# Kernel optimization log

Measured on AMD Instinct MI355X. Metric: run time of the kernel, lower is better.

The kernel has to match this reference:

```python
import jax, jax.numpy as jnp
import numpy as np
from jax import lax

B, N, CIN, COUT, NPOINT, K = 8, 4096, 64, 128, 1024, 24
EPS = 1e-5


def setup_inputs() -> dict:
    key = jax.random.key(0)
    ks = jax.random.split(key, 16)
    def conv_w(k, o, i):
        return jax.random.normal(k, (o, i), jnp.float32) * (1.0 / np.sqrt(i))
    inp = {
        "xyz": jax.random.normal(ks[0], (B, N, 3), jnp.float32),
        "x": jax.random.normal(ks[1], (B, CIN, N), jnp.float32),
        "farthest0": jax.random.randint(ks[2], (B,), 0, N),
        # Local.proj: Conv1DBR (CIN -> COUT, k=1, no bias)
        "W_proj": conv_w(ks[3], COUT, CIN), "g_proj": jnp.ones(COUT), "b_proj": jnp.zeros(COUT),
        # Local.channel: one Conv1DBRRes (COUT -> COUT -> COUT)
        "W_la1": conv_w(ks[4], COUT, COUT), "g_la1": jnp.ones(COUT), "b_la1": jnp.zeros(COUT),
        "W_la2": conv_w(ks[5], COUT, COUT), "g_la2": jnp.ones(COUT), "b_la2": jnp.zeros(COUT),
        # ca: one Conv1DBRRes (COUT -> COUT -> COUT)
        "W_ca1": conv_w(ks[6], COUT, COUT), "g_ca1": jnp.ones(COUT), "b_ca1": jnp.zeros(COUT),
        "W_ca2": conv_w(ks[7], COUT, COUT), "g_ca2": jnp.ones(COUT), "b_ca2": jnp.zeros(COUT),
    }
    return inp


def _bn(z, g, b):
    # BatchNorm1d in training mode: biased batch stats over (batch, length)
    mu = z.mean((0, 2), keepdims=True)
    var = z.var((0, 2), keepdims=True)
    return g[None, :, None] * (z - mu) * lax.rsqrt(var + EPS) + b[None, :, None]


def _conv(z, W):  # kernel_size=1 Conv1d == channel matmul
    return jnp.einsum('oc,mcl->mol', W, z)


def _resblock(z, W1, g1, b1, W2, g2, b2):
    y = jax.nn.relu(_bn(_conv(z, W1), g1, b1))
    y = _bn(_conv(y, W2), g2, b2)
    return jax.nn.relu(y + z)


def _forward(xyz, x, farthest0,
             W_proj, g_proj, b_proj,
             W_la1, g_la1, b_la1, W_la2, g_la2, b_la2,
             W_ca1, g_ca1, b_ca1, W_ca2, g_ca2, b_ca2):
    Bv, Nv, _ = xyz.shape
    xt = jnp.transpose(x, (0, 2, 1))  # [B, N, C]

    # --- farthest point sampling (sequential, vectorized over batch) ---
    def step(carry, _):
        dist, far = carry
        c = jnp.take_along_axis(xyz, far[:, None, None], axis=1)  # [B,1,3]
        d = jnp.sum((xyz - c) ** 2, -1)                           # [B,N]
        dist = jnp.minimum(dist, d)
        return (dist, jnp.argmax(dist, -1)), far

    init = (jnp.full((Bv, Nv), 1e10, xyz.dtype), farthest0)
    _, cent = lax.scan(step, init, None, length=NPOINT)
    fps_idx = cent.T  # [B, NPOINT]

    new_xyz = jnp.take_along_axis(xyz, fps_idx[:, :, None], axis=1)  # [B,NP,3]
    new_pts = jnp.take_along_axis(xt, fps_idx[:, :, None], axis=1)   # [B,NP,C]

    # --- kNN grouping: squared distances [B, NP, N], smallest-K indices ---
    d2 = (jnp.sum(new_xyz ** 2, -1)[:, :, None]
          + jnp.sum(xyz ** 2, -1)[:, None, :]
          - 2.0 * jnp.einsum('bpc,bnc->bpn', new_xyz, xyz))
    _, knn = lax.top_k(-d2, K)  # [B, NP, K]
    grouped = jax.vmap(lambda p, i: p[i])(xt, knn)  # [B, NP, K, C]
    edge = grouped - new_pts[:, :, None, :]         # [B, NP, K, C]

    # --- Local: per-group conv-BN-ReLU + residual block + max over K ---
    M = Bv * NPOINT
    h = jnp.transpose(edge, (0, 1, 3, 2)).reshape(M, edge.shape[-1], K)  # [M, CIN, K]
    h = jax.nn.relu(_bn(_conv(h, W_proj), g_proj, b_proj))
    h = _resblock(h, W_la1, g_la1, b_la1, W_la2, g_la2, b_la2)
    h = h.max(-1)  # adaptive_max_pool1d(.,1) -> [M, COUT]
    h = h.reshape(Bv, NPOINT, -1).transpose(0, 2, 1)  # [B, COUT, NP]

    # --- Channel (ca) ---
    h = _resblock(h, W_ca1, g_ca1, b_ca1, W_ca2, g_ca2, b_ca2)
    return new_xyz, h


def reference(xyz, x, farthest0,
              W_proj, g_proj, b_proj,
              W_la1, g_la1, b_la1, W_la2, g_la2, b_la2,
              W_ca1, g_ca1, b_ca1, W_ca2, g_ca2, b_ca2):
    return _forward(xyz, x, farthest0,
                    W_proj, g_proj, b_proj,
                    W_la1, g_la1, b_la1, W_la2, g_la2, b_la2,
                    W_ca1, g_ca1, b_ca1, W_ca2, g_ca2, b_ca2)
```

## Files before the change

kernel.cpp:

```cpp
#include <hip/hip_runtime.h>

#define BB 8
#define NN 4096
#define CIN 64
#define COUTC 128
#define NPT 1024
#define KNN 24

typedef unsigned short u16;
typedef unsigned int u32;
typedef unsigned long long u64;

using short8v = __attribute__((ext_vector_type(8))) short;
using f32x4  = __attribute__((ext_vector_type(4))) float;
using f32x2  = __attribute__((ext_vector_type(2))) float;

__device__ __forceinline__ u16 f2bf(float f){ u32 u=__float_as_uint(f); u += 0x7FFFu + ((u>>16)&1u); return (u16)(u>>16); }
__device__ __forceinline__ float bf2f(u16 h){ return __uint_as_float(((u32)h)<<16); }

template<int C> __device__ __forceinline__ float dppmax_f32(float x){
  int y=__builtin_amdgcn_update_dpp(__float_as_int(x),__float_as_int(x),C,0xF,0xF,false);
  return fmaxf(x,__int_as_float(y));
}
template<int C> __device__ __forceinline__ u32 dppmin_u32(u32 x){
  u32 y=(u32)__builtin_amdgcn_update_dpp((int)x,(int)x,C,0xF,0xF,false);
  return y<x?y:x;
}
__device__ __forceinline__ f32x2 vmin2(f32x2 a, f32x2 b){
#if __has_builtin(__builtin_elementwise_min)
  return __builtin_elementwise_min(a,b);
#else
  f32x2 r; r.x=fminf(a.x,b.x); r.y=fminf(a.y,b.y); return r;
#endif
}
__device__ __forceinline__ f32x2 vmax2(f32x2 a, f32x2 b){
#if __has_builtin(__builtin_elementwise_max)
  return __builtin_elementwise_max(a,b);
#else
  f32x2 r; r.x=fmaxf(a.x,b.x); r.y=fmaxf(a.y,b.y); return r;
#endif
}

__global__ __launch_bounds__(256) void xt_kern(const float* __restrict__ x, float* __restrict__ xt,
                                               const float* __restrict__ xyz, float* __restrict__ sn){
  __shared__ float tile[64][68];
  int blk=blockIdx.x; int b=blk>>6; int n0=(blk&63)<<6;
  int t=threadIdx.x;
  {
    int c=t>>2, nj=(t&3)*16;
    const float4* gp=reinterpret_cast<const float4*>(x + ((size_t)(b*64+c))*NN + n0+nj);
    #pragma unroll
    for(int j=0;j<4;j++){
      float4 v=gp[j];
      *reinterpret_cast<float4*>(&tile[c][nj+4*j])=v;
    }
  }
  if(t<64){
    int n=n0+t;
    const float* p=xyz+((size_t)b*NN+n)*3;
    float xx=p[0], yy=p[1], zz=p[2];
    sn[b*NN+n]=__fadd_rn(__fadd_rn(__fmul_rn(xx,xx),__fmul_rn(yy,yy)),__fmul_rn(zz,zz));
  }
  __syncthreads();
  {
    int n=t>>2, c16=(t&3)*16;
    size_t base=((size_t)(b*NN+n0+n))*64 + c16;
    #pragma unroll
    for(int j=0;j<4;j++){
      *reinterpret_cast<float4*>(xt+base+4*j)=
        make_float4(tile[c16+4*j][n],tile[c16+4*j+1][n],tile[c16+4*j+2][n],tile[c16+4*j+3][n]);
    }
  }
}

__global__ __launch_bounds__(256) void fps_kern(const float* __restrict__ xyz,
    const int* __restrict__ far0, int* __restrict__ fps_idx)
{
  __shared__ float4 lp[NN];
  __shared__ u64 mkey[2][4];
  const int b=blockIdx.x, t=threadIdx.x, w=t>>6, l=t&63;
  f32x2 px2[8],py2[8],pz2[8],d2v[8];
  {
    float4 q[12];
    const float4* gp=reinterpret_cast<const float4*>(xyz+(size_t)b*NN*3)+(size_t)t*12;
    #pragma unroll
    for(int i=0;i<12;i++) q[i]=gp[i];
    const float* v=reinterpret_cast<const float*>(q);
    #pragma unroll
    for(int j=0;j<8;j++){
      px2[j]=(f32x2){v[6*j+0],v[6*j+3]};
      py2[j]=(f32x2){v[6*j+1],v[6*j+4]};
      pz2[j]=(f32x2){v[6*j+2],v[6*j+5]};
      lp[t*16+2*j  ]=make_float4(v[6*j+0],v[6*j+1],v[6*j+2],0.f);
      lp[t*16+2*j+1]=make_float4(v[6*j+3],v[6*j+4],v[6*j+5],0.f);
      d2v[j]=(f32x2){1e10f,1e10f};
    }
  }
  __syncthreads();
  int far=far0[b];
  float4 c=lp[far];
  int par=0;
  for(int it=0;it<NPT;++it){
    if(t==0) fps_idx[b*NPT+it]=far;
    f32x2 cx2=(f32x2){c.x,c.x}, cy2=(f32x2){c.y,c.y}, cz2=(f32x2){c.z,c.z};
    f32x2 m2=(f32x2){-1.f,-1.f};
    #pragma unroll
    for(int j=0;j<8;j++){
      f32x2 dx=px2[j]-cx2, dy=py2[j]-cy2, dz=pz2[j]-cz2;
      f32x2 d=(dx*dx+dy*dy)+dz*dz;
      f32x2 nd=vmin2(d2v[j],d); d2v[j]=nd;
      m2=vmax2(m2,nd);
    }
    float m0=fmaxf(m2.x,m2.y);
    if(it==NPT-1) break;
    float r=m0;
    r=dppmax_f32<0x111>(r); r=dppmax_f32<0x112>(r); r=dppmax_f32<0x114>(r);
    r=dppmax_f32<0x118>(r); r=dppmax_f32<0x142>(r); r=dppmax_f32<0x143>(r);
    float wmax=__int_as_float(__builtin_amdgcn_readlane(__float_as_int(r),63));
    u64 bal=__ballot(m0==wmax);
    int winlane=__ffsll((unsigned long long)bal)-1;
    int myj=15;
    #pragma unroll
    for(int j=7;j>=0;--j){
      if(d2v[j].y==m0) myj=2*j+1;
      if(d2v[j].x==m0) myj=2*j;
    }
    int widx_w=__builtin_amdgcn_readlane(t*16+myj,winlane);
    if(l==0) mkey[par][w]=(((u64)__float_as_uint(wmax))<<32)|(u32)(~(u32)widx_w);
    asm volatile("s_waitcnt lgkmcnt(0)\n\ts_barrier" ::: "memory");
    u64 k4=mkey[par][l&3];
    u32 klo=(u32)k4, khi=(u32)(k4>>32);
    {
      u32 nlo=(u32)__builtin_amdgcn_update_dpp((int)klo,(int)klo,0xB1,0xF,0xF,false);
      u32 nhi=(u32)__builtin_amdgcn_update_dpp((int)khi,(int)khi,0xB1,0xF,0xF,false);
      bool g=(nhi>khi)||((nhi==khi)&&(nlo>klo));
      klo=g?nlo:klo; khi=g?nhi:khi;
    }
    {
      u32 nlo=(u32)__builtin_amdgcn_update_dpp((int)klo,(int)klo,0x4E,0xF,0xF,false);
      u32 nhi=(u32)__builtin_amdgcn_update_dpp((int)khi,(int)khi,0x4E,0xF,0xF,false);
      bool g=(nhi>khi)||((nhi==khi)&&(nlo>klo));
      klo=g?nlo:klo; khi=g?nhi:khi;
    }
    int widx=(int)(~klo);
    far=widx;
    c=lp[widx];
    par^=1;
  }
}

__global__ __launch_bounds__(256) void knn_kern(const float* __restrict__ xyz,
  const float* __restrict__ sn, const int* __restrict__ fps,
  const float* __restrict__ xt, u16* __restrict__ edge, float* __restrict__ outxyz)
{
  __shared__ u64 mkey[2][4];
  __shared__ int sel[KNN];
  const int m=blockIdx.x, b=m>>10;
  const int t=threadIdx.x, w=t>>6, l=t&63;
  const int ctr=fps[m];
  const float sp=sn[b*NN+ctr];
  float cx,cy,cz;
  { const float* cp=xyz+((size_t)b*NN+ctr)*3; cx=cp[0]; cy=cp[1]; cz=cp[2]; }
  u32 key[16];
  {
    float4 q[12];
    const float4* gp=reinterpret_cast<const float4*>(xyz+((size_t)b*NN)*3+(size_t)t*48);
    #pragma unroll
    for(int i=0;i<12;i++) q[i]=gp[i];
    const float* v=reinterpret_cast<const float*>(q);
    float snl[16];
    const float4* sp4=reinterpret_cast<const float4*>(sn+b*NN+t*16);
    #pragma unroll
    for(int i=0;i<4;i++){ float4 s4=sp4[i]; snl[4*i]=s4.x; snl[4*i+1]=s4.y; snl[4*i+2]=s4.z; snl[4*i+3]=s4.w; }
    #pragma unroll
    for(int j=0;j<16;j++){
      float nx=v[3*j], ny=v[3*j+1], nz=v[3*j+2];
      float dot=__fadd_rn(__fadd_rn(__fmul_rn(cx,nx),__fmul_rn(cy,ny)),__fmul_rn(cz,nz));
      float d2=__fsub_rn(__fadd_rn(sp,snl[j]),__fmul_rn(2.f,dot));
      u32 bbv=__float_as_uint(d2);
      key[j]=(bbv&0x80000000u)?~bbv:(bbv|0x80000000u);
    }
  }
  u32 loc=0xFFFFFFFFu; int myj=0;
  #pragma unroll
  for(int j=15;j>=0;--j){ if(key[j]<=loc){ loc=key[j]; myj=j; } }
  int par=0;
  for(int rd=0;rd<KNN;rd++){
    u32 r=loc;
    r=dppmin_u32<0x111>(r); r=dppmin_u32<0x112>(r); r=dppmin_u32<0x114>(r);
    r=dppmin_u32<0x118>(r); r=dppmin_u32<0x142>(r); r=dppmin_u32<0x143>(r);
    u32 wmin=(u32)__builtin_amdgcn_readlane((int)r,63);
    u64 bal=__ballot(loc==wmin);
    int winlane=__ffsll((unsigned long long)bal)-1;
    int widx_w=__builtin_amdgcn_readlane(t*16+myj,winlane);
    if(l==0) mkey[par][w]=(((u64)wmin)<<32)|(u32)widx_w;
    asm volatile("s_waitcnt lgkmcnt(0)\n\ts_barrier" ::: "memory");
    u64 b0=mkey[par][0],b1=mkey[par][1],b2=mkey[par][2],b3=mkey[par][3];
    u64 bb0=b0<b1?b0:b1, bb1=b2<b3?b2:b3, best=bb0<bb1?bb0:bb1;
    int widx=(int)(u32)(best&0xFFFFFFFFull);
    if(t==(widx>>4)){
      key[widx&15]=0xFFFFFFFFu;
      loc=0xFFFFFFFFu; myj=0;
      #pragma unroll
      for(int j=15;j>=0;--j){ if(key[j]<=loc){ loc=key[j]; myj=j; } }
    }
    if(t==0) sel[rd]=widx;
    par^=1;
  }
  if(t<3) outxyz[(size_t)m*3+t]=xyz[((size_t)b*NN+ctr)*3+t];
  __syncthreads();
  {
    int r=t>>3, c0=(t&7)*8;
    if(r<KNN){
      int nb=sel[r];
      const float* np_=xt+((size_t)b*NN+nb)*64+c0;
      const float* cp_=xt+((size_t)b*NN+ctr)*64+c0;
      float4 n0=*reinterpret_cast<const float4*>(np_);
      float4 n1=*reinterpret_cast<const float4*>(np_+4);
      float4 c0v=*reinterpret_cast<const float4*>(cp_);
      float4 c1v=*reinterpret_cast<const float4*>(cp_+4);
      u32 ov[4];
      ov[0]=(u32)f2bf(__fsub_rn(n0.x,c0v.x))|((u32)f2bf(__fsub_rn(n0.y,c0v.y))<<16);
      ov[1]=(u32)f2bf(__fsub_rn(n0.z,c0v.z))|((u32)f2bf(__fsub_rn(n0.w,c0v.w))<<16);
      ov[2]=(u32)f2bf(__fsub_rn(n1.x,c1v.x))|((u32)f2bf(__fsub_rn(n1.y,c1v.y))<<16);
      ov[3]=(u32)f2bf(__fsub_rn(n1.z,c1v.z))|((u32)f2bf(__fsub_rn(n1.w,c1v.w))<<16);
      *reinterpret_cast<uint4*>(edge+((size_t)m*KNN+r)*64+c0)=make_uint4(ov[0],ov[1],ov[2],ov[3]);
    }
  }
}

template<int KD, bool XF>
__global__ __launch_bounds__(256) void gemm_bn(
    const u16* __restrict__ A, const float* __restrict__ W,
    const float* __restrict__ af, const float* __restrict__ cf,
    u16* __restrict__ Z, float* __restrict__ pSum, float* __restrict__ pSq,
    int nblk4)
{
  extern __shared__ char smem[];
  u16* lA=(u16*)smem;
  u16* lW=lA+128*KD;
  const int t=threadIdx.x, blk=blockIdx.x;
  constexpr int TPR=KD/8;
  constexpr int RPP=256/TPR;
  constexpr int NPASS=128/RPP;
  const int rl=t/TPR, c0=(t%TPR)*8;
  float ax[8], cxx[8];
  if constexpr (XF){
    #pragma unroll
    for(int j=0;j<8;j++){ ax[j]=af[c0+j]; cxx[j]=cf[c0+j]; }
  }
  #pragma unroll
  for(int p=0;p<NPASS;p++){
    int row=p*RPP+rl;
    uint4 v=*reinterpret_cast<const uint4*>(A+((size_t)blk*128+row)*KD+c0);
    if constexpr (XF){
      u32 in[4]={v.x,v.y,v.z,v.w}; u32 out[4];
      #pragma unroll
      for(int q2=0;q2<4;q2++){
        float f0=__uint_as_float((in[q2]&0xFFFFu)<<16);
        float f1=__uint_as_float(in[q2]&0xFFFF0000u);
        f0=fmaxf(fmaf(ax[2*q2],f0,cxx[2*q2]),0.f);
        f1=fmaxf(fmaf(ax[2*q2+1],f1,cxx[2*q2+1]),0.f);
        out[q2]=(u32)f2bf(f0)|((u32)f2bf(f1)<<16);
      }
      v.x=out[0]; v.y=out[1]; v.z=out[2]; v.w=out[3];
    }
    int byte=row*(KD*2)+c0*2; byte^=(row&7)<<4;
    *reinterpret_cast<uint4*>((char*)lA+byte)=v;
    const float* wp_=W+(size_t)row*KD+c0;
    float4 w0=*reinterpret_cast<const float4*>(wp_);
    float4 w1=*reinterpret_cast<const float4*>(wp_+4);
    uint4 wv;
    wv.x=(u32)f2bf(w0.x)|((u32)f2bf(w0.y)<<16);
    wv.y=(u32)f2bf(w0.z)|((u32)f2bf(w0.w)<<16);
    wv.z=(u32)f2bf(w1.x)|((u32)f2bf(w1.y)<<16);
    wv.w=(u32)f2bf(w1.z)|((u32)f2bf(w1.w)<<16);
    int wbyte=row*(KD*2)+c0*2; wbyte^=(row&7)<<4;
    *reinterpret_cast<uint4*>((char*)lW+wbyte)=wv;
  }
  __syncthreads();
  const int l=t&63, w2=t>>6;
  const int l15=l&15, qq=l>>4;
  f32x4 acc[2][8];
  #pragma unroll
  for(int r=0;r<2;r++)
    #pragma unroll
    for(int f=0;f<8;f++) acc[r][f]=(f32x4){0.f,0.f,0.f,0.f};
  #pragma unroll
  for(int s=0;s<KD/32;s++){
    short8v a[2];
    #pragma unroll
    for(int r=0;r<2;r++){
      int row=w2*32+r*16+l15;
      int byte=row*(KD*2)+s*64+qq*16; byte^=(row&7)<<4;
      a[r]=*reinterpret_cast<const short8v*>((char*)lA+byte);
    }
    #pragma unroll
    for(int f=0;f<8;f++){
      int row=f*16+l15;
      int byte=row*(KD*2)+s*64+qq*16; byte^=(row&7)<<4;
      short8v bb=*reinterpret_cast<const short8v*>((char*)lW+byte);
      acc[0][f]=__builtin_amdgcn_mfma_f32_16x16x32_bf16(a[0],bb,acc[0][f],0,0,0);
      acc[1][f]=__builtin_amdgcn_mfma_f32_16x16x32_bf16(a[1],bb,acc[1][f],0,0,0);
    }
  }
  #pragma unroll
  for(int f=0;f<8;f++){
    float sv=0.f,qv=0.f;
    #pragma unroll
    for(int r=0;r<2;r++){
      int grow=blk*128+w2*32+r*16+qq*4;
      #pragma unroll
      for(int j=0;j<4;j++){
        float v=acc[r][f][j];
        Z[((size_t)(grow+j))*128+f*16+l15]=f2bf(v);
        sv+=v; qv+=v*v;
      }
    }
    sv+=__shfl_xor(sv,16); sv+=__shfl_xor(sv,32);
    qv+=__shfl_xor(qv,16); qv+=__shfl_xor(qv,32);
    if(l<16){
      int col=f*16+l15;
      pSum[(size_t)col*nblk4+blk*4+w2]=sv;
      pSq [(size_t)col*nblk4+blk*4+w2]=qv;
    }
  }
}

__global__ __launch_bounds__(256) void stats_kern(
  const float* __restrict__ pSum, const float* __restrict__ pSq,
  const float* __restrict__ g, const float* __restrict__ bb,
  float* __restrict__ af, float* __restrict__ cf, int nparts, float inv_cnt)
{
  int ch=blockIdx.x, t=threadIdx.x;
  float s=0.f,q=0.f;
  for(int i=t;i<nparts;i+=256){ s+=pSum[(size_t)ch*nparts+i]; q+=pSq[(size_t)ch*nparts+i]; }
  #pragma unroll
  for(int o=1;o<64;o<<=1){ s+=__shfl_xor(s,o); q+=__shfl_xor(q,o); }
  __shared__ float ls[4], lq[4];
  int w=t>>6, l=t&63;
  if(l==0){ ls[w]=s; lq[w]=q; }
  __syncthreads();
  if(t==0){
    float S=ls[0]+ls[1]+ls[2]+ls[3], Q=lq[0]+lq[1]+lq[2]+lq[3];
    float mu=S*inv_cnt, var=Q*inv_cnt-mu*mu;
    float a=g[ch]/sqrtf(var+1e-5f);
    af[ch]=a; cf[ch]=bb[ch]-mu*a;
  }
}

__global__ __launch_bounds__(256) void pool_kern(const u16* __restrict__ z3, const u16* __restrict__ z1,
  const float* __restrict__ af1, const float* __restrict__ cf1,
  const float* __restrict__ af3, const float* __restrict__ cf3, u16* __restrict__ pooled)
{
  int t=threadIdx.x;
  int g=blockIdx.x*2+(t>>7);
  int c=t&127;
  float a1=af1[c],c1=cf1[c],a3=af3[c],c3=cf3[c];
  float mmax=0.f;
  size_t base=(size_t)g*KNN*128+c;
  #pragma unroll 4
  for(int k=0;k<KNN;k++){
    float v3=bf2f(z3[base+(size_t)k*128]);
    float v1=bf2f(z1[base+(size_t)k*128]);
    float z1p=fmaxf(fmaf(a1,v1,c1),0.f);
    float v=fmaf(a3,v3,c3)+z1p;
    mmax=fmaxf(mmax,fmaxf(v,0.f));
  }
  pooled[(size_t)g*128+c]=f2bf(mmax);
}

__global__ __launch_bounds__(256) void final_kern(const u16* __restrict__ z5,
  const u16* __restrict__ pooled, const float* __restrict__ af, const float* __restrict__ cf,
  float* __restrict__ outh)
{
  __shared__ float tile[64][68];
  int blk=blockIdx.x; int b=blk>>5; int tl=blk&31; int p0=(tl&15)<<6; int o0=(tl>>4)<<6;
  int t=threadIdx.x;
  {
    int pl=t>>2, o1=(t&3)*16;
    size_t base=((size_t)(b*1024+p0+pl))*128 + o0+o1;
    #pragma unroll
    for(int h2=0;h2<2;h2++){
      uint4 v5=*reinterpret_cast<const uint4*>(z5+base+h2*8);
      uint4 vp=*reinterpret_cast<const uint4*>(pooled+base+h2*8);
      u32 a5[4]={v5.x,v5.y,v5.z,v5.w}; u32 pp[4]={vp.x,vp.y,vp.z,vp.w};
      #pragma unroll
      for(int q2=0;q2<4;q2++){
        int oj=o1+h2*8+q2*2;
        float g0=af[o0+oj],h0=cf[o0+oj],g1=af[o0+oj+1],h1=cf[o0+oj+1];
        float f0=__uint_as_float((a5[q2]&0xFFFFu)<<16);
        float f1=__uint_as_float(a5[q2]&0xFFFF0000u);
        float q0=__uint_as_float((pp[q2]&0xFFFFu)<<16);
        float q1=__uint_as_float(pp[q2]&0xFFFF0000u);
        tile[oj][pl]  =fmaxf(fmaf(g0,f0,h0)+q0,0.f);
        tile[oj+1][pl]=fmaxf(fmaf(g1,f1,h1)+q1,0.f);
      }
    }
  }
  __syncthreads();
  {
    int ol=t>>2, pj=(t&3)*16;
    size_t obase=((size_t)(b*128+o0+ol))*1024 + p0+pj;
    #pragma unroll
    for(int j=0;j<4;j++){
      *reinterpret_cast<float4*>(outh+obase+4*j)=
        make_float4(tile[ol][pj+4*j],tile[ol][pj+4*j+1],tile[ol][pj+4*j+2],tile[ol][pj+4*j+3]);
    }
  }
}

extern "C" void kernel_launch(void* const* d_in, const int* in_sizes, int n_in,
                              void* d_out, int out_size, void* d_ws, size_t ws_size,
                              hipStream_t stream)
{
  (void)in_sizes; (void)n_in; (void)out_size; (void)ws_size;
  const float* xyz   =(const float*)d_in[0];
  const float* x     =(const float*)d_in[1];
  const int*   far0  =(const int*)d_in[2];
  const float* W_proj=(const float*)d_in[3];
  const float* g_proj=(const float*)d_in[4];
  const float* b_proj=(const float*)d_in[5];
  const float* W_la1 =(const float*)d_in[6];
  const float* g_la1 =(const float*)d_in[7];
  const float* b_la1 =(const float*)d_in[8];
  const float* W_la2 =(const float*)d_in[9];
  const float* g_la2 =(const float*)d_in[10];
  const float* b_la2 =(const float*)d_in[11];
  const float* W_ca1 =(const float*)d_in[12];
  const float* g_ca1 =(const float*)d_in[13];
  const float* b_ca1 =(const float*)d_in[14];
  const float* W_ca2 =(const float*)d_in[15];
  const float* g_ca2 =(const float*)d_in[16];
  const float* b_ca2 =(const float*)d_in[17];

  char* ws=(char*)d_ws;
  const size_t OFF_XT =0;
  const size_t OFF_SN =8388608;
  const size_t OFF_FPS=8519680;
  const size_t OFF_AF =8552448;
  const size_t OFF_CF =8555008;
  const size_t OFF_PS =8557568;
  const size_t OFF_PQ =11703296;
  const size_t OFF_PL =14849024;
  const size_t OFF_Z4 =16946176;
  const size_t OFF_Z5 =19043328;
  const size_t OFF_Z1 =21140480;
  const size_t OFF_B2 =71472128;

  float* xt  =(float*)(ws+OFF_XT);
  float* sn  =(float*)(ws+OFF_SN);
  int* fps   =(int*)(ws+OFF_FPS);
  float* af  =(float*)(ws+OFF_AF);
  float* cf  =(float*)(ws+OFF_CF);
  float* pS  =(float*)(ws+OFF_PS);
  float* pQ  =(float*)(ws+OFF_PQ);
  u16* pooled=(u16*)(ws+OFF_PL);
  u16* z4    =(u16*)(ws+OFF_Z4);
  u16* z5    =(u16*)(ws+OFF_Z5);
  u16* z1    =(u16*)(ws+OFF_Z1);
  u16* edge  =(u16*)(ws+OFF_B2);
  u16* z2    =(u16*)(ws+OFF_B2);
  u16* z3    =(u16*)(ws+OFF_B2);
  float* outxyz=(float*)d_out;
  float* outh  =(float*)d_out+24576;

  const float invL=1.f/196608.f, invC=1.f/8192.f;

  xt_kern<<<512,256,0,stream>>>(x,xt,xyz,sn);
  fps_kern<<<8,256,0,stream>>>(xyz,far0,fps);
  knn_kern<<<8192,256,0,stream>>>(xyz,sn,fps,xt,edge,outxyz);

  gemm_bn<64,false><<<1536,256,32768,stream>>>(edge,W_proj,nullptr,nullptr,z1,pS,pQ,6144);
  stats_kern<<<128,256,0,stream>>>(pS,pQ,g_proj,b_proj,af+0,cf+0,6144,invL);

  gemm_bn<128,true><<<1536,256,65536,stream>>>(z1,W_la1,af+0,cf+0,z2,pS,pQ,6144);
  stats_kern<<<128,256,0,stream>>>(pS,pQ,g_la1,b_la1,af+128,cf+128,6144,invL);

  gemm_bn<128,true><<<1536,256,65536,stream>>>(z2,W_la2,af+128,cf+128,z3,pS,pQ,6144);
  stats_kern<<<128,256,0,stream>>>(pS,pQ,g_la2,b_la2,af+256,cf+256,6144,invL);

  pool_kern<<<4096,256,0,stream>>>(z3,z1,af+0,cf+0,af+256,cf+256,pooled);

  gemm_bn<128,false><<<64,256,65536,stream>>>(pooled,W_ca1,nullptr,nullptr,z4,pS,pQ,256);
  stats_kern<<<128,256,0,stream>>>(pS,pQ,g_ca1,b_ca1,af+384,cf+384,256,invC);

  gemm_bn<128,true><<<64,256,65536,stream>>>(z4,W_ca2,af+384,cf+384,z5,pS,pQ,256);
  stats_kern<<<128,256,0,stream>>>(pS,pQ,g_ca2,b_ca2,af+512,cf+512,256,invC);

  final_kern<<<256,256,0,stream>>>(z5,pooled,af+512,cf+512,outh);
}
```

Measured before the change: 835.3 us.

## Merge transpose into FPS launch and make kNN selection barrier-free per wave

The transpose/norm kernel and the FPS kernel are merged into one launch. FPS runs in blocks 0-7 and the transpose tiles in the remaining blocks, reusing FPS's shared array as the tile. In kNN, each wave independently extracts its own top-24 candidates without a block barrier per round. A final merge step then ranks the 4x24 candidates by binary search to pick the global top-24. This removes 24 block-wide barriers per kNN block and one kernel launch, at the cost of each wave doing 24 rounds regardless and an extra merge phase.

```diff
diff --git a/kernel.cpp b/kernel.cpp
--- a/kernel.cpp
+++ b/kernel.cpp
@@ -41,44 +41,44 @@
 #endif
 }
 
-__global__ __launch_bounds__(256) void xt_kern(const float* __restrict__ x, float* __restrict__ xt,
-                                               const float* __restrict__ xyz, float* __restrict__ sn){
-  __shared__ float tile[64][68];
-  int blk=blockIdx.x; int b=blk>>6; int n0=(blk&63)<<6;
-  int t=threadIdx.x;
-  {
-    int c=t>>2, nj=(t&3)*16;
-    const float4* gp=reinterpret_cast<const float4*>(x + ((size_t)(b*64+c))*NN + n0+nj);
-    #pragma unroll
-    for(int j=0;j<4;j++){
-      float4 v=gp[j];
-      *reinterpret_cast<float4*>(&tile[c][nj+4*j])=v;
-    }
-  }
-  if(t<64){
-    int n=n0+t;
-    const float* p=xyz+((size_t)b*NN+n)*3;
-    float xx=p[0], yy=p[1], zz=p[2];
-    sn[b*NN+n]=__fadd_rn(__fadd_rn(__fmul_rn(xx,xx),__fmul_rn(yy,yy)),__fmul_rn(zz,zz));
-  }
-  __syncthreads();
-  {
-    int n=t>>2, c16=(t&3)*16;
-    size_t base=((size_t)(b*NN+n0+n))*64 + c16;
-    #pragma unroll
-    for(int j=0;j<4;j++){
-      *reinterpret_cast<float4*>(xt+base+4*j)=
-        make_float4(tile[c16+4*j][n],tile[c16+4*j+1][n],tile[c16+4*j+2][n],tile[c16+4*j+3][n]);
-    }
-  }
-}
-
-__global__ __launch_bounds__(256) void fps_kern(const float* __restrict__ xyz,
+__global__ __launch_bounds__(256) void pre_kern(const float* __restrict__ x, float* __restrict__ xt,
+    const float* __restrict__ xyz, float* __restrict__ sn,
     const int* __restrict__ far0, int* __restrict__ fps_idx)
 {
   __shared__ float4 lp[NN];
   __shared__ u64 mkey[2][4];
-  const int b=blockIdx.x, t=threadIdx.x, w=t>>6, l=t&63;
+  const int t=threadIdx.x;
+  if(blockIdx.x>=8){
+    float (*tile)[68]=reinterpret_cast<float(*)[68]>(lp);
+    int blk=blockIdx.x-8; int b=blk>>6; int n0=(blk&63)<<6;
+    {
+      int c=t>>2, nj=(t&3)*16;
+      const float4* gp=reinterpret_cast<const float4*>(x + ((size_t)(b*64+c))*NN + n0+nj);
+      #pragma unroll
+      for(int j=0;j<4;j++){
+        float4 v=gp[j];
+        *reinterpret_cast<float4*>(&tile[c][nj+4*j])=v;
+      }
+    }
+    if(t<64){
+      int n=n0+t;
+      const float* p=xyz+((size_t)b*NN+n)*3;
+      float xx=p[0], yy=p[1], zz=p[2];
+      sn[b*NN+n]=__fadd_rn(__fadd_rn(__fmul_rn(xx,xx),__fmul_rn(yy,yy)),__fmul_rn(zz,zz));
+    }
+    __syncthreads();
+    {
+      int n=t>>2, c16=(t&3)*16;
+      size_t base=((size_t)(b*NN+n0+n))*64 + c16;
+      #pragma unroll
+      for(int j=0;j<4;j++){
+        *reinterpret_cast<float4*>(xt+base+4*j)=
+          make_float4(tile[c16+4*j][n],tile[c16+4*j+1][n],tile[c16+4*j+2][n],tile[c16+4*j+3][n]);
+      }
+    }
+    return;
+  }
+  const int b=blockIdx.x, w=t>>6, l=t&63;
   f32x2 px2[8],py2[8],pz2[8],d2v[8];
   {
     float4 q[12];
@@ -153,7 +153,8 @@
   const float* __restrict__ sn, const int* __restrict__ fps,
   const float* __restrict__ xt, u16* __restrict__ edge, float* __restrict__ outxyz)
 {
-  __shared__ u64 mkey[2][4];
+  __shared__ u32 ckey[4][KNN];
+  __shared__ int cidx[4][KNN];
   __shared__ int sel[KNN];
   const int m=blockIdx.x, b=m>>10;
   const int t=threadIdx.x, w=t>>6, l=t&63;
@@ -184,7 +185,6 @@
   u32 loc=0xFFFFFFFFu; int myj=0;
   #pragma unroll
   for(int j=15;j>=0;--j){ if(key[j]<=loc){ loc=key[j]; myj=j; } }
-  int par=0;
   for(int rd=0;rd<KNN;rd++){
     u32 r=loc;
     r=dppmin_u32<0x111>(r); r=dppmin_u32<0x112>(r); r=dppmin_u32<0x114>(r);
@@ -193,19 +193,31 @@
     u64 bal=__ballot(loc==wmin);
     int winlane=__ffsll((unsigned long long)bal)-1;
     int widx_w=__builtin_amdgcn_readlane(t*16+myj,winlane);
-    if(l==0) mkey[par][w]=(((u64)wmin)<<32)|(u32)widx_w;
-    asm volatile("s_waitcnt lgkmcnt(0)\n\ts_barrier" ::: "memory");
-    u64 b0=mkey[par][0],b1=mkey[par][1],b2=mkey[par][2],b3=mkey[par][3];
-    u64 bb0=b0<b1?b0:b1, bb1=b2<b3?b2:b3, best=bb0<bb1?bb0:bb1;
-    int widx=(int)(u32)(best&0xFFFFFFFFull);
-    if(t==(widx>>4)){
-      key[widx&15]=0xFFFFFFFFu;
+    if(l==winlane){
+      key[myj]=0xFFFFFFFFu;
       loc=0xFFFFFFFFu; myj=0;
       #pragma unroll
       for(int j=15;j>=0;--j){ if(key[j]<=loc){ loc=key[j]; myj=j; } }
     }
-    if(t==0) sel[rd]=widx;
-    par^=1;
+    if(l==0){ ckey[w][rd]=wmin; cidx[w][rd]=widx_w; }
+  }
+  __syncthreads();
+  if(t<96){
+    int wl=t/24, i=t-wl*24;
+    u32 k=ckey[wl][i]; int idx=cidx[wl][i];
+    int rank=i;
+    #pragma unroll
+    for(int ww=0;ww<4;ww++){
+      if(ww==wl) continue;
+      int lo=0,hi=KNN;
+      while(lo<hi){ int mid=(lo+hi)>>1;
+        u32 k2=ckey[ww][mid]; int i2=cidx[ww][mid];
+        bool less=(k2<k)||(k2==k&&i2<idx);
+        if(less) lo=mid+1; else hi=mid;
+      }
+      rank+=lo;
+    }
+    if(rank<KNN) sel[rank]=idx;
   }
   if(t<3) outxyz[(size_t)m*3+t]=xyz[((size_t)b*NN+ctr)*3+t];
   __syncthreads();
@@ -467,8 +479,7 @@
 
   const float invL=1.f/196608.f, invC=1.f/8192.f;
 
-  xt_kern<<<512,256,0,stream>>>(x,xt,xyz,sn);
-  fps_kern<<<8,256,0,stream>>>(xyz,far0,fps);
+  pre_kern<<<520,256,0,stream>>>(x,xt,xyz,sn,far0,fps);
   knn_kern<<<8192,256,0,stream>>>(xyz,sn,fps,xt,edge,outxyz);
 
   gemm_bn<64,false><<<1536,256,32768,stream>>>(edge,W_proj,nullptr,nullptr,z1,pS,pQ,6144);
```

Result: slower. 892.6 us (+6.9%).

## Fuse transpose, FPS and kNN into one persistent kernel with flag-based overlap

Applied to the files above, without the earlier changes.

Merges the transpose/norm, farthest point sampling and kNN/edge-gather kernels into one 512-block launch. Eight blocks run FPS and publish each sampled index through an atomic store. The other 504 worker blocks first do the transpose, meet at a global atomic barrier, then spin on per-sample flags so kNN for early centroids overlaps with the sequential FPS. This hides the kNN work behind the long serial FPS chain, at the cost of spin-waiting, two extra memsets, and relying on all 512 blocks being resident at once.

```diff
diff --git a/kernel.cpp b/kernel.cpp
--- a/kernel.cpp
+++ b/kernel.cpp
@@ -6,6 +6,7 @@
 #define COUTC 128
 #define NPT 1024
 #define KNN 24
+#define NWRK 504
 
 typedef unsigned short u16;
 typedef unsigned int u32;
@@ -41,44 +42,139 @@
 #endif
 }
 
-__global__ __launch_bounds__(256) void xt_kern(const float* __restrict__ x, float* __restrict__ xt,
-                                               const float* __restrict__ xyz, float* __restrict__ sn){
-  __shared__ float tile[64][68];
-  int blk=blockIdx.x; int b=blk>>6; int n0=(blk&63)<<6;
-  int t=threadIdx.x;
-  {
-    int c=t>>2, nj=(t&3)*16;
-    const float4* gp=reinterpret_cast<const float4*>(x + ((size_t)(b*64+c))*NN + n0+nj);
-    #pragma unroll
-    for(int j=0;j<4;j++){
-      float4 v=gp[j];
-      *reinterpret_cast<float4*>(&tile[c][nj+4*j])=v;
-    }
-  }
-  if(t<64){
-    int n=n0+t;
-    const float* p=xyz+((size_t)b*NN+n)*3;
-    float xx=p[0], yy=p[1], zz=p[2];
-    sn[b*NN+n]=__fadd_rn(__fadd_rn(__fmul_rn(xx,xx),__fmul_rn(yy,yy)),__fmul_rn(zz,zz));
-  }
-  __syncthreads();
-  {
-    int n=t>>2, c16=(t&3)*16;
-    size_t base=((size_t)(b*NN+n0+n))*64 + c16;
-    #pragma unroll
-    for(int j=0;j<4;j++){
-      *reinterpret_cast<float4*>(xt+base+4*j)=
-        make_float4(tile[c16+4*j][n],tile[c16+4*j+1][n],tile[c16+4*j+2][n],tile[c16+4*j+3][n]);
-    }
-  }
-}
-
-__global__ __launch_bounds__(256) void fps_kern(const float* __restrict__ xyz,
-    const int* __restrict__ far0, int* __restrict__ fps_idx)
+__global__ __launch_bounds__(256) void pre_kern(const float* __restrict__ x, float* __restrict__ xt,
+    const float* __restrict__ xyz, float* __restrict__ sn,
+    const int* __restrict__ far0, int* fps_idx, int* sync,
+    u16* __restrict__ edge, float* __restrict__ outxyz)
 {
   __shared__ float4 lp[NN];
   __shared__ u64 mkey[2][4];
-  const int b=blockIdx.x, t=threadIdx.x, w=t>>6, l=t&63;
+  __shared__ int sel[KNN];
+  __shared__ int bcast;
+  const int t=threadIdx.x;
+  if(blockIdx.x>=8){
+    const int blk0=blockIdx.x-8;
+    float (*tile)[68]=reinterpret_cast<float(*)[68]>(lp);
+    for(int tl=blk0; tl<512; tl+=NWRK){
+      int b=tl>>6, n0=(tl&63)<<6;
+      {
+        int c=t>>2, nj=(t&3)*16;
+        const float4* gp=reinterpret_cast<const float4*>(x + ((size_t)(b*64+c))*NN + n0+nj);
+        #pragma unroll
+        for(int j=0;j<4;j++){
+          float4 v=gp[j];
+          *reinterpret_cast<float4*>(&tile[c][nj+4*j])=v;
+        }
+      }
+      if(t<64){
+        int n=n0+t;
+        const float* p=xyz+((size_t)b*NN+n)*3;
+        float xx=p[0], yy=p[1], zz=p[2];
+        sn[b*NN+n]=__fadd_rn(__fadd_rn(__fmul_rn(xx,xx),__fmul_rn(yy,yy)),__fmul_rn(zz,zz));
+      }
+      __syncthreads();
+      {
+        int n=t>>2, c16=(t&3)*16;
+        size_t base=((size_t)(b*NN+n0+n))*64 + c16;
+        #pragma unroll
+        for(int j=0;j<4;j++){
+          *reinterpret_cast<float4*>(xt+base+4*j)=
+            make_float4(tile[c16+4*j][n],tile[c16+4*j+1][n],tile[c16+4*j+2][n],tile[c16+4*j+3][n]);
+        }
+      }
+      __syncthreads();
+    }
+    if(t==0){
+      __hip_atomic_fetch_add(sync,1,__ATOMIC_RELEASE,__HIP_MEMORY_SCOPE_AGENT);
+      while(__hip_atomic_load(sync,__ATOMIC_ACQUIRE,__HIP_MEMORY_SCOPE_AGENT)<NWRK)
+        __builtin_amdgcn_s_sleep(8);
+    }
+    __syncthreads();
+    const int w=t>>6, l=t&63;
+    for(int m=blk0; m<8192; m+=NWRK){
+      if(t==0){
+        int v;
+        while((v=__hip_atomic_load(&fps_idx[m],__ATOMIC_RELAXED,__HIP_MEMORY_SCOPE_AGENT))<0)
+          __builtin_amdgcn_s_sleep(8);
+        bcast=v;
+      }
+      __syncthreads();
+      const int ctr=bcast;
+      const int b=m>>10;
+      const float sp=sn[b*NN+ctr];
+      float cx,cy,cz;
+      { const float* cp=xyz+((size_t)b*NN+ctr)*3; cx=cp[0]; cy=cp[1]; cz=cp[2]; }
+      u32 key[16];
+      {
+        float4 q[12];
+        const float4* gp=reinterpret_cast<const float4*>(xyz+((size_t)b*NN)*3+(size_t)t*48);
+        #pragma unroll
+        for(int i=0;i<12;i++) q[i]=gp[i];
+        const float* v=reinterpret_cast<const float*>(q);
+        float snl[16];
+        const float4* sp4=reinterpret_cast<const float4*>(sn+b*NN+t*16);
+        #pragma unroll
+        for(int i=0;i<4;i++){ float4 s4=sp4[i]; snl[4*i]=s4.x; snl[4*i+1]=s4.y; snl[4*i+2]=s4.z; snl[4*i+3]=s4.w; }
+        #pragma unroll
+        for(int j=0;j<16;j++){
+          float nx=v[3*j], ny=v[3*j+1], nz=v[3*j+2];
+          float dot=__fadd_rn(__fadd_rn(__fmul_rn(cx,nx),__fmul_rn(cy,ny)),__fmul_rn(cz,nz));
+          float d2=__fsub_rn(__fadd_rn(sp,snl[j]),__fmul_rn(2.f,dot));
+          u32 bbv=__float_as_uint(d2);
+          key[j]=(bbv&0x80000000u)?~bbv:(bbv|0x80000000u);
+        }
+      }
+      u32 loc=0xFFFFFFFFu; int myj=0;
+      #pragma unroll
+      for(int j=15;j>=0;--j){ if(key[j]<=loc){ loc=key[j]; myj=j; } }
+      int par=0;
+      for(int rd=0;rd<KNN;rd++){
+        u32 r=loc;
+        r=dppmin_u32<0x111>(r); r=dppmin_u32<0x112>(r); r=dppmin_u32<0x114>(r);
+        r=dppmin_u32<0x118>(r); r=dppmin_u32<0x142>(r); r=dppmin_u32<0x143>(r);
+        u32 wmin=(u32)__builtin_amdgcn_readlane((int)r,63);
+        u64 bal=__ballot(loc==wmin);
+        int winlane=__ffsll((unsigned long long)bal)-1;
+        int widx_w=__builtin_amdgcn_readlane(t*16+myj,winlane);
+        if(l==0) mkey[par][w]=(((u64)wmin)<<32)|(u32)widx_w;
+        asm volatile("s_waitcnt lgkmcnt(0)\n\ts_barrier" ::: "memory");
+        u64 b0=mkey[par][0],b1=mkey[par][1],b2=mkey[par][2],b3=mkey[par][3];
+        u64 bb0=b0<b1?b0:b1, bb1=b2<b3?b2:b3, best=bb0<bb1?bb0:bb1;
+        int widx=(int)(u32)(best&0xFFFFFFFFull);
+        if(t==(widx>>4)){
+          key[widx&15]=0xFFFFFFFFu;
+          loc=0xFFFFFFFFu; myj=0;
+          #pragma unroll
+          for(int j=15;j>=0;--j){ if(key[j]<=loc){ loc=key[j]; myj=j; } }
+        }
+        if(t==0) sel[rd]=widx;
+        par^=1;
+      }
+      if(t<3) outxyz[(size_t)m*3+t]=xyz[((size_t)b*NN+ctr)*3+t];
+      __syncthreads();
+      {
+        int r2=t>>3, c0=(t&7)*8;
+        if(r2<KNN){
+          int nb=sel[r2];
+          const float* np_=xt+((size_t)b*NN+nb)*64+c0;
+          const float* cp_=xt+((size_t)b*NN+ctr)*64+c0;
+          float4 n0=*reinterpret_cast<const float4*>(np_);
+          float4 n1=*reinterpret_cast<const float4*>(np_+4);
+          float4 c0v=*reinterpret_cast<const float4*>(cp_);
+          float4 c1v=*reinterpret_cast<const float4*>(cp_+4);
+          u32 ov[4];
+          ov[0]=(u32)f2bf(__fsub_rn(n0.x,c0v.x))|((u32)f2bf(__fsub_rn(n0.y,c0v.y))<<16);
+          ov[1]=(u32)f2bf(__fsub_rn(n0.z,c0v.z))|((u32)f2bf(__fsub_rn(n0.w,c0v.w))<<16);
+          ov[2]=(u32)f2bf(__fsub_rn(n1.x,c1v.x))|((u32)f2bf(__fsub_rn(n1.y,c1v.y))<<16);
+          ov[3]=(u32)f2bf(__fsub_rn(n1.z,c1v.z))|((u32)f2bf(__fsub_rn(n1.w,c1v.w))<<16);
+          *reinterpret_cast<uint4*>(edge+((size_t)m*KNN+r2)*64+c0)=make_uint4(ov[0],ov[1],ov[2],ov[3]);
+        }
+      }
+      __syncthreads();
+    }
+    return;
+  }
+  const int b=blockIdx.x, w=t>>6, l=t&63;
   f32x2 px2[8],py2[8],pz2[8],d2v[8];
   {
     float4 q[12];
@@ -101,7 +197,7 @@
   float4 c=lp[far];
   int par=0;
   for(int it=0;it<NPT;++it){
-    if(t==0) fps_idx[b*NPT+it]=far;
+    if(t==0) __hip_atomic_store(&fps_idx[b*NPT+it],far,__ATOMIC_RELAXED,__HIP_MEMORY_SCOPE_AGENT);
     f32x2 cx2=(f32x2){c.x,c.x}, cy2=(f32x2){c.y,c.y}, cz2=(f32x2){c.z,c.z};
     f32x2 m2=(f32x2){-1.f,-1.f};
     #pragma unroll
@@ -146,86 +242,6 @@
     far=widx;
     c=lp[widx];
     par^=1;
-  }
-}
-
-__global__ __launch_bounds__(256) void knn_kern(const float* __restrict__ xyz,
-  const float* __restrict__ sn, const int* __restrict__ fps,
-  const float* __restrict__ xt, u16* __restrict__ edge, float* __restrict__ outxyz)
-{
-  __shared__ u64 mkey[2][4];
-  __shared__ int sel[KNN];
-  const int m=blockIdx.x, b=m>>10;
-  const int t=threadIdx.x, w=t>>6, l=t&63;
-  const int ctr=fps[m];
-  const float sp=sn[b*NN+ctr];
-  float cx,cy,cz;
-  { const float* cp=xyz+((size_t)b*NN+ctr)*3; cx=cp[0]; cy=cp[1]; cz=cp[2]; }
-  u32 key[16];
-  {
-    float4 q[12];
-    const float4* gp=reinterpret_cast<const float4*>(xyz+((size_t)b*NN)*3+(size_t)t*48);
-    #pragma unroll
-    for(int i=0;i<12;i++) q[i]=gp[i];
-    const float* v=reinterpret_cast<const float*>(q);
-    float snl[16];
-    const float4* sp4=reinterpret_cast<const float4*>(sn+b*NN+t*16);
-    #pragma unroll
-    for(int i=0;i<4;i++){ float4 s4=sp4[i]; snl[4*i]=s4.x; snl[4*i+1]=s4.y; snl[4*i+2]=s4.z; snl[4*i+3]=s4.w; }
-    #pragma unroll
-    for(int j=0;j<16;j++){
-      float nx=v[3*j], ny=v[3*j+1], nz=v[3*j+2];
-      float dot=__fadd_rn(__fadd_rn(__fmul_rn(cx,nx),__fmul_rn(cy,ny)),__fmul_rn(cz,nz));
-      float d2=__fsub_rn(__fadd_rn(sp,snl[j]),__fmul_rn(2.f,dot));
-      u32 bbv=__float_as_uint(d2);
-      key[j]=(bbv&0x80000000u)?~bbv:(bbv|0x80000000u);
-    }
-  }
-  u32 loc=0xFFFFFFFFu; int myj=0;
-  #pragma unroll
-  for(int j=15;j>=0;--j){ if(key[j]<=loc){ loc=key[j]; myj=j; } }
-  int par=0;
-  for(int rd=0;rd<KNN;rd++){
-    u32 r=loc;
-    r=dppmin_u32<0x111>(r); r=dppmin_u32<0x112>(r); r=dppmin_u32<0x114>(r);
-    r=dppmin_u32<0x118>(r); r=dppmin_u32<0x142>(r); r=dppmin_u32<0x143>(r);
-    u32 wmin=(u32)__builtin_amdgcn_readlane((int)r,63);
-    u64 bal=__ballot(loc==wmin);
-    int winlane=__ffsll((unsigned long long)bal)-1;
-    int widx_w=__builtin_amdgcn_readlane(t*16+myj,winlane);
-    if(l==0) mkey[par][w]=(((u64)wmin)<<32)|(u32)widx_w;
-    asm volatile("s_waitcnt lgkmcnt(0)\n\ts_barrier" ::: "memory");
-    u64 b0=mkey[par][0],b1=mkey[par][1],b2=mkey[par][2],b3=mkey[par][3];
-    u64 bb0=b0<b1?b0:b1, bb1=b2<b3?b2:b3, best=bb0<bb1?bb0:bb1;
-    int widx=(int)(u32)(best&0xFFFFFFFFull);
-    if(t==(widx>>4)){
-      key[widx&15]=0xFFFFFFFFu;
-      loc=0xFFFFFFFFu; myj=0;
-      #pragma unroll
-      for(int j=15;j>=0;--j){ if(key[j]<=loc){ loc=key[j]; myj=j; } }
-    }
-    if(t==0) sel[rd]=widx;
-    par^=1;
-  }
-  if(t<3) outxyz[(size_t)m*3+t]=xyz[((size_t)b*NN+ctr)*3+t];
-  __syncthreads();
-  {
-    int r=t>>3, c0=(t&7)*8;
-    if(r<KNN){
-      int nb=sel[r];
-      const float* np_=xt+((size_t)b*NN+nb)*64+c0;
-      const float* cp_=xt+((size_t)b*NN+ctr)*64+c0;
-      float4 n0=*reinterpret_cast<const float4*>(np_);
-      float4 n1=*reinterpret_cast<const float4*>(np_+4);
-      float4 c0v=*reinterpret_cast<const float4*>(cp_);
-      float4 c1v=*reinterpret_cast<const float4*>(cp_+4);
-      u32 ov[4];
-      ov[0]=(u32)f2bf(__fsub_rn(n0.x,c0v.x))|((u32)f2bf(__fsub_rn(n0.y,c0v.y))<<16);
-      ov[1]=(u32)f2bf(__fsub_rn(n0.z,c0v.z))|((u32)f2bf(__fsub_rn(n0.w,c0v.w))<<16);
-      ov[2]=(u32)f2bf(__fsub_rn(n1.x,c1v.x))|((u32)f2bf(__fsub_rn(n1.y,c1v.y))<<16);
-      ov[3]=(u32)f2bf(__fsub_rn(n1.z,c1v.z))|((u32)f2bf(__fsub_rn(n1.w,c1v.w))<<16);
-      *reinterpret_cast<uint4*>(edge+((size_t)m*KNN+r)*64+c0)=make_uint4(ov[0],ov[1],ov[2],ov[3]);
-    }
   }
 }
 
@@ -438,19 +454,21 @@
   const size_t OFF_XT =0;
   const size_t OFF_SN =8388608;
   const size_t OFF_FPS=8519680;
-  const size_t OFF_AF =8552448;
-  const size_t OFF_CF =8555008;
-  const size_t OFF_PS =8557568;
-  const size_t OFF_PQ =11703296;
-  const size_t OFF_PL =14849024;
-  const size_t OFF_Z4 =16946176;
-  const size_t OFF_Z5 =19043328;
-  const size_t OFF_Z1 =21140480;
-  const size_t OFF_B2 =71472128;
+  const size_t OFF_SY =8552448;
+  const size_t OFF_AF =8552704;
+  const size_t OFF_CF =8555264;
+  const size_t OFF_PS =8557824;
+  const size_t OFF_PQ =11703552;
+  const size_t OFF_PL =14849280;
+  const size_t OFF_Z4 =16946432;
+  const size_t OFF_Z5 =19043584;
+  const size_t OFF_Z1 =21140736;
+  const size_t OFF_B2 =71472384;
 
   float* xt  =(float*)(ws+OFF_XT);
   float* sn  =(float*)(ws+OFF_SN);
   int* fps   =(int*)(ws+OFF_FPS);
+  int* sync  =(int*)(ws+OFF_SY);
   float* af  =(float*)(ws+OFF_AF);
   float* cf  =(float*)(ws+OFF_CF);
   float* pS  =(float*)(ws+OFF_PS);
@@ -467,9 +485,10 @@
 
   const float invL=1.f/196608.f, invC=1.f/8192.f;
 
-  xt_kern<<<512,256,0,stream>>>(x,xt,xyz,sn);
-  fps_kern<<<8,256,0,stream>>>(xyz,far0,fps);
-  knn_kern<<<8192,256,0,stream>>>(xyz,sn,fps,xt,edge,outxyz);
+  hipMemsetAsync(fps,0xFF,NPT*BB*sizeof(int),stream);
+  hipMemsetAsync(sync,0,sizeof(int),stream);
+
+  pre_kern<<<512,256,0,stream>>>(x,xt,xyz,sn,far0,fps,sync,edge,outxyz);
 
   gemm_bn<64,false><<<1536,256,32768,stream>>>(edge,W_proj,nullptr,nullptr,z1,pS,pQ,6144);
   stats_kern<<<128,256,0,stream>>>(pS,pQ,g_proj,b_proj,af+0,cf+0,6144,invL);
```

After: 939.6 us. 1.12x slower.
